# Kernel tuning notes

Hardware: AMD Instinct MI355X
Metric: run time of the kernel (lower is better)

The kernel has to match this reference:

```python
import jax, jax.numpy as jnp
import numpy as np

# Hardcoded in the torch module: interpolate to size=(32, 64) -> H=32, W=64
OUT_H, OUT_W = 32, 64
IGNORE_LABEL = 19
TAU = 0.07
EPS = 1e-12  # F.normalize eps


def _lin_idx(in_size, out_size):
    # torch bilinear, align_corners=False (default): half-pixel centers, clamped
    src = (jnp.arange(out_size, dtype=jnp.float32) + 0.5) * (in_size / out_size) - 0.5
    src = jnp.clip(src, 0.0, in_size - 1)
    i0 = jnp.floor(src).astype(jnp.int32)
    i1 = jnp.minimum(i0 + 1, in_size - 1)
    w = src - i0.astype(jnp.float32)
    return i0, i1, w


def bilinear_resize(x, Ho, Wo):
    # x: [B, C, Hi, Wi] -> [B, C, Ho, Wo], separable lerp
    Hi, Wi = x.shape[2], x.shape[3]
    h0, h1, wh = _lin_idx(Hi, Ho)
    w0, w1, ww = _lin_idx(Wi, Wo)
    wh = wh[None, None, :, None]
    xh = x[:, :, h0, :] * (1.0 - wh) + x[:, :, h1, :] * wh
    return xh[:, :, :, w0] * (1.0 - ww) + xh[:, :, :, w1] * ww


def nearest_resize_labels(lab, Ho, Wo):
    # torch 'nearest' (legacy): src = floor(dst * in/out)
    Hi, Wi = lab.shape[1], lab.shape[2]
    ih = jnp.floor(jnp.arange(Ho) * (Hi / Ho)).astype(jnp.int32)
    iw = jnp.floor(jnp.arange(Wo) * (Wi / Wo)).astype(jnp.int32)
    return lab[:, ih, :][:, :, iw]


def setup_inputs() -> dict:
    key = jax.random.key(0)
    k1, k2 = jax.random.split(key)
    features = jax.random.normal(k1, (8, 256, 128, 256), dtype=jnp.float32)
    labels = jax.random.randint(k2, (8, 128, 256), 0, 20, dtype=jnp.int32)
    return {"features": features, "labels": labels}


def reference(features, labels):
    # --- forward() ---
    f = bilinear_resize(features, OUT_H, OUT_W)               # [B, C, 32, 64]
    lab = nearest_resize_labels(labels, OUT_H, OUT_W)         # [B, 32, 64]
    lab = lab.astype(jnp.float32).reshape(lab.shape[0], -1)   # [B, N], N=2048

    B, C = f.shape[0], f.shape[1]
    f = f.reshape(B, C, -1).transpose(0, 2, 1)                # [B, N, C]
    f = f / jnp.maximum(jnp.linalg.norm(f, axis=2, keepdims=True), EPS)

    eq = (lab[:, :, None] == lab[:, None, :])                 # [B, N, N]
    ign = (lab == IGNORE_LABEL).astype(f.dtype)               # [B, N]
    weight_mask = eq.astype(f.dtype) * (1.0 - ign[:, :, None])
    ign_t = ign[:, None, :]                                   # ignore_mask_t (cols)

    logits = jnp.einsum('bnc,bmc->bnm', f, f) / TAU           # [B, N, N]
    # NOTE: original code computes a -1e9-masked copy but passes the UNMASKED
    # logits into supervised_contrastive_loss; we reproduce that faithfully.

    # --- supervised_contrastive_loss() ---
    p = jax.nn.softmax(logits, axis=2)
    p = p * (1.0 - ign_t) + ign_t                             # ignored cols -> 1 (log 0)
    ll = jnp.sum(-jnp.log(p) * weight_mask, axis=2)           # [B, N]
    den = jnp.sum(weight_mask, axis=2)                        # [B, N]
    ind = (den == 0).astype(f.dtype)
    den = den * (1.0 - ind) + ind
    ll = ll / den
    ll = jnp.where(jnp.isnan(ll), 0.0, ll)                    # nan -> 0
    index_sum = jnp.sum(1.0 - ind, axis=1)                    # [B]
    ind2 = (index_sum == 0).astype(f.dtype)
    index_sum = index_sum + ind2
    loss = jnp.mean(jnp.sum(ll, axis=1) / index_sum)
    return loss
```

## Files before the change

### kernel.cpp

```cpp
#include <hip/hip_runtime.h>
#include <math.h>

#define NB 8
#define NC 256
#define HI 128
#define WI 256
#define NN 2048
#define IGN 19
#define SQT 3.7796447300922722f

typedef _Float16 half8  __attribute__((ext_vector_type(8)));
typedef _Float16 half4v __attribute__((ext_vector_type(4)));
typedef float    f32x4  __attribute__((ext_vector_type(4)));

#define MFMA16(a, b, c) __builtin_amdgcn_mfma_f32_16x16x32_f16((a), (b), (c), 0, 0, 0)
#define GLOAD_LDS16(gp, lp) __builtin_amdgcn_global_load_lds( \
    (const __attribute__((address_space(1))) void*)(gp), \
    (__attribute__((address_space(3))) void*)(lp), 16, 0, 0)

__global__ void k_resize(const float* __restrict__ x, float* __restrict__ G) {
    int t = blockIdx.x * 256 + threadIdx.x;
    int j = t & 63;
    int i = (t >> 6) & 31;
    int c = (t >> 11) & 255;
    int b = t >> 19;
    const float* row = x + ((((size_t)b*NC + c)*HI + (4*i+1))*WI + 4*j);
    float4 r0 = *(const float4*)row;
    float4 r1 = *(const float4*)(row + WI);
    G[((size_t)b*NC + c)*NN + i*64 + j] = 0.25f*(r0.y + r0.z + r1.y + r1.z);
}

__global__ void k_labels(const int* __restrict__ lab, int* __restrict__ L,
                         int* __restrict__ hist) {
    int b = blockIdx.x;
    __shared__ int h[20];
    if (threadIdx.x < 20) h[threadIdx.x] = 0;
    __syncthreads();
    for (int n = threadIdx.x; n < NN; n += 256) {
        int i = n >> 6, j = n & 63;
        int v = lab[((size_t)b*HI + 4*i)*WI + 4*j];
        L[b*NN + n] = v;
        atomicAdd(&h[v], 1);
    }
    __syncthreads();
    if (threadIdx.x < 20) hist[b*20 + threadIdx.x] = h[threadIdx.x];
}

__global__ void k_norm(const float* __restrict__ G, float* __restrict__ invn) {
    int t = blockIdx.x * 256 + threadIdx.x;
    int b = t >> 11, n = t & 2047;
    const float* p = G + (size_t)b*NC*NN + n;
    float s = 0.f;
    #pragma unroll 8
    for (int c = 0; c < NC; c++) { float v = p[c*NN]; s += v*v; }
    invn[t] = 1.0f / fmaxf(sqrtf(s), 1e-12f);
}

__global__ void k_pack(const float* __restrict__ G, const float* __restrict__ invn,
                       _Float16* __restrict__ Phi, _Float16* __restrict__ Plo) {
    int blk = blockIdx.x;
    int b  = blk & 7;
    int t  = blk >> 3;
    int c0 = (t >> 5) * 64;
    int n0 = (t & 31) * 64;
    __shared__ float T[64][65];
    const float* Gb = G + (size_t)b*NC*NN;
    const float* invb = invn + b*NN;
    int tid = threadIdx.x;
    #pragma unroll
    for (int it = 0; it < 4; it++) {
        int idx = it*256 + tid;
        int cl = idx >> 4, nq = idx & 15;
        float4 v = *(const float4*)&Gb[(size_t)(c0+cl)*NN + n0 + nq*4];
        T[cl][nq*4+0]=v.x; T[cl][nq*4+1]=v.y; T[cl][nq*4+2]=v.z; T[cl][nq*4+3]=v.w;
    }
    __syncthreads();
    #pragma unroll
    for (int it = 0; it < 4; it++) {
        int idx = it*256 + tid;
        int nl = idx >> 4, cq = idx & 15;
        float s = invb[n0+nl] * SQT;
        half4v hh, hl;
        #pragma unroll
        for (int e = 0; e < 4; e++) {
            float v = T[cq*4+e][nl] * s;
            _Float16 h = (_Float16)v;
            hh[e] = h;
            hl[e] = (_Float16)(v - (float)h);
        }
        size_t o = ((size_t)(b*NN + n0 + nl))*NC + c0 + cq*4;
        *(half4v*)&Phi[o] = hh;
        *(half4v*)&Plo[o] = hl;
    }
}

__global__ __launch_bounds__(256, 1)
void k_main(const _Float16* __restrict__ Phi, const _Float16* __restrict__ Plo,
            const int* __restrict__ L, const int* __restrict__ hist,
            float* __restrict__ rowval) {
    int b    = blockIdx.x & 7;
    int tile = blockIdx.x >> 3;
    int n0   = tile * 64;
    const _Float16* PhiB = Phi + (size_t)b*NN*NC;
    const _Float16* PloB = Plo + (size_t)b*NN*NC;
    const int* Lb = L + b*NN;

    __shared__ _Float16 BhS[2][64*NC];
    __shared__ _Float16 BlS[2][64*NC];
    __shared__ float smM[2][64], smS[2][64], smMS[2][64];

    int tid  = threadIdx.x;
    int lane = tid & 63;
    int w    = tid >> 6;
    int wr   = w >> 1, wc = w & 1;
    int lr16 = lane & 15, lq = lane >> 4;

    half8 Ah[2][8], Al[2][8];
    #pragma unroll
    for (int t = 0; t < 2; t++) {
        int row = n0 + wr*32 + t*16 + lr16;
        const _Float16* pa = PhiB + (size_t)row*NC + lq*8;
        const _Float16* pb = PloB + (size_t)row*NC + lq*8;
        #pragma unroll
        for (int s = 0; s < 8; s++) {
            Ah[t][s] = *(const half8*)(pa + s*32);
            Al[t][s] = *(const half8*)(pb + s*32);
        }
    }
    int4 lr4[2];
    #pragma unroll
    for (int t = 0; t < 2; t++)
        lr4[t] = *(const int4*)&Lb[n0 + wr*32 + t*16 + lq*4];

    float sm_m[8], sm_s[8], sm_ms[8];
    #pragma unroll
    for (int i = 0; i < 8; i++) { sm_m[i] = -1e30f; sm_s[i] = 0.f; sm_ms[i] = 0.f; }

    auto stage = [&](int mt, int buf) {
        int mb = mt * 64;
        #pragma unroll
        for (int it = 0; it < 8; it++) {
            int ch  = w*512 + it*64 + lane;
            int col = ch >> 5, kbs = ch & 31;
            int src = (mb + col)*NC + ((kbs ^ (col & 7)) << 3);
            int dst = (w*512 + it*64) * 8;
            GLOAD_LDS16(PhiB + src, &BhS[buf][dst]);
            GLOAD_LDS16(PloB + src, &BlS[buf][dst]);
        }
    };

    auto compute = [&](int mt, int buf) {
        int mb  = mt * 64;
        int cl0 = wc*32 + lr16;
        int cl1 = cl0 + 16;
        int lc0 = Lb[mb + cl0];
        int lc1 = Lb[mb + cl1];
        f32x4 acc[2][2];
        #pragma unroll
        for (int t = 0; t < 2; t++)
            #pragma unroll
            for (int u = 0; u < 2; u++) acc[t][u] = (f32x4){0.f,0.f,0.f,0.f};

        #pragma unroll
        for (int s = 0; s < 8; s++) {
            int x0 = ((s*4 + lq) ^ (lr16 & 7)) << 3;
            half8 B0h = *(const half8*)&BhS[buf][cl0*NC + x0];
            half8 B1h = *(const half8*)&BhS[buf][cl1*NC + x0];
            half8 B0l = *(const half8*)&BlS[buf][cl0*NC + x0];
            half8 B1l = *(const half8*)&BlS[buf][cl1*NC + x0];
            #pragma unroll
            for (int t = 0; t < 2; t++) {
                acc[t][0] = MFMA16(Ah[t][s], B0h, acc[t][0]);
                acc[t][0] = MFMA16(Ah[t][s], B0l, acc[t][0]);
                acc[t][0] = MFMA16(Al[t][s], B0h, acc[t][0]);
                acc[t][1] = MFMA16(Ah[t][s], B1h, acc[t][1]);
                acc[t][1] = MFMA16(Ah[t][s], B1l, acc[t][1]);
                acc[t][1] = MFMA16(Al[t][s], B1h, acc[t][1]);
            }
        }
        #pragma unroll
        for (int t = 0; t < 2; t++) {
            int lrv[4] = {lr4[t].x, lr4[t].y, lr4[t].z, lr4[t].w};
            #pragma unroll
            for (int r = 0; r < 4; r++) {
                float v0 = acc[t][0][r], v1 = acc[t][1][r];
                int i = t*4 + r;
                float nm = fmaxf(sm_m[i], fmaxf(v0, v1));
                sm_s[i] = sm_s[i]*__expf(sm_m[i]-nm) + __expf(v0-nm) + __expf(v1-nm);
                sm_m[i] = nm;
                sm_ms[i] += (lc0 == lrv[r] ? v0 : 0.f) + (lc1 == lrv[r] ? v1 : 0.f);
            }
        }
    };

    stage(0, 0);
    __syncthreads();
    for (int mt = 0; mt < 32; mt++) {
        int cur = mt & 1;
        if (mt + 1 < 32) stage(mt + 1, cur ^ 1);
        compute(mt, cur);
        __syncthreads();
    }

    #pragma unroll
    for (int i = 0; i < 8; i++) {
        #pragma unroll
        for (int off = 1; off < 16; off <<= 1) {
            float om  = __shfl_xor(sm_m[i], off, 16);
            float os  = __shfl_xor(sm_s[i], off, 16);
            float oms = __shfl_xor(sm_ms[i], off, 16);
            float nm = fmaxf(sm_m[i], om);
            sm_s[i] = sm_s[i]*__expf(sm_m[i]-nm) + os*__expf(om-nm);
            sm_m[i] = nm;
            sm_ms[i] += oms;
        }
    }
    if (lr16 == 0) {
        #pragma unroll
        for (int t = 0; t < 2; t++)
            #pragma unroll
            for (int r = 0; r < 4; r++) {
                int rl = wr*32 + t*16 + lq*4 + r;
                smM[wc][rl]  = sm_m[t*4+r];
                smS[wc][rl]  = sm_s[t*4+r];
                smMS[wc][rl] = sm_ms[t*4+r];
            }
    }
    __syncthreads();
    if (tid < 64) {
        float m0 = smM[0][tid], m1 = smM[1][tid];
        float nm = fmaxf(m0, m1);
        float ss = smS[0][tid]*__expf(m0-nm) + smS[1][tid]*__expf(m1-nm);
        float msv = smMS[0][tid] + smMS[1][tid];
        int lrv = Lb[n0 + tid];
        float o = 0.f;
        if (lrv != IGN) {
            float den = (float)hist[b*20 + lrv];
            o = (nm + logf(ss)) - msv/den;
        }
        rowval[b*NN + n0 + tid] = o;
    }
}

__global__ void k_final(const float* __restrict__ rowval,
                        const int* __restrict__ hist, float* __restrict__ out) {
    __shared__ float red[4];
    int tid = threadIdx.x;
    float loss = 0.f;
    for (int b = 0; b < NB; b++) {
        float s = 0.f;
        for (int n = tid; n < NN; n += 256) s += rowval[b*NN + n];
        #pragma unroll
        for (int off = 32; off >= 1; off >>= 1) s += __shfl_down(s, off, 64);
        if ((tid & 63) == 0) red[tid >> 6] = s;
        __syncthreads();
        if (tid == 0) {
            float tot = red[0] + red[1] + red[2] + red[3];
            int cnt = NN - hist[b*20 + IGN];
            float isum = (cnt == 0) ? 1.f : (float)cnt;
            loss += tot / isum;
        }
        __syncthreads();
    }
    if (tid == 0) out[0] = loss / (float)NB;
}

extern "C" void kernel_launch(void* const* d_in, const int* in_sizes, int n_in,
                              void* d_out, int out_size, void* d_ws, size_t ws_size,
                              hipStream_t stream) {
    const float* x  = (const float*)d_in[0];
    const int* lab  = (const int*)d_in[1];
    float* out      = (float*)d_out;
    char* ws        = (char*)d_ws;

    const size_t G_BYTES = (size_t)NB*NC*NN*4;
    const size_t P_BYTES = (size_t)NB*NC*NN*2;
    float*     G      = (float*)ws;
    _Float16*  Phi    = (_Float16*)(ws + G_BYTES);
    _Float16*  Plo    = (_Float16*)(ws + G_BYTES + P_BYTES);
    float*     invn   = (float*)(ws + G_BYTES + 2*P_BYTES);
    float*     rowval = (float*)(ws + G_BYTES + 2*P_BYTES + 65536);
    int*       L      = (int*)  (ws + G_BYTES + 2*P_BYTES + 2*65536);
    int*       hist   = (int*)  (ws + G_BYTES + 2*P_BYTES + 3*65536);

    k_resize<<<NB*NC*NN/256, 256, 0, stream>>>(x, G);
    k_labels<<<NB, 256, 0, stream>>>(lab, L, hist);
    k_norm  <<<NB*NN/256, 256, 0, stream>>>(G, invn);
    k_pack  <<<NB*4*32, 256, 0, stream>>>(G, invn, Phi, Plo);
    k_main  <<<NB*(NN/64), 256, 0, stream>>>(Phi, Plo, L, hist, rowval);
    k_final <<<1, 256, 0, stream>>>(rowval, hist, out);
}
```

Before: 433.6 us.

## Fuse resize, norm and fp16 split-pack into one kernel; atomically reduce row losses

```diff
diff --git a/kernel.cpp b/kernel.cpp
--- a/kernel.cpp
+++ b/kernel.cpp
@@ -10,7 +10,6 @@
 #define SQT 3.7796447300922722f
 
 typedef _Float16 half8  __attribute__((ext_vector_type(8)));
-typedef _Float16 half4v __attribute__((ext_vector_type(4)));
 typedef float    f32x4  __attribute__((ext_vector_type(4)));
 
 #define MFMA16(a, b, c) __builtin_amdgcn_mfma_f32_16x16x32_f16((a), (b), (c), 0, 0, 0)
@@ -18,23 +17,12 @@
     (const __attribute__((address_space(1))) void*)(gp), \
     (__attribute__((address_space(3))) void*)(lp), 16, 0, 0)
 
-__global__ void k_resize(const float* __restrict__ x, float* __restrict__ G) {
-    int t = blockIdx.x * 256 + threadIdx.x;
-    int j = t & 63;
-    int i = (t >> 6) & 31;
-    int c = (t >> 11) & 255;
-    int b = t >> 19;
-    const float* row = x + ((((size_t)b*NC + c)*HI + (4*i+1))*WI + 4*j);
-    float4 r0 = *(const float4*)row;
-    float4 r1 = *(const float4*)(row + WI);
-    G[((size_t)b*NC + c)*NN + i*64 + j] = 0.25f*(r0.y + r0.z + r1.y + r1.z);
-}
-
 __global__ void k_labels(const int* __restrict__ lab, int* __restrict__ L,
-                         int* __restrict__ hist) {
+                         int* __restrict__ hist, float* __restrict__ accB) {
     int b = blockIdx.x;
     __shared__ int h[20];
     if (threadIdx.x < 20) h[threadIdx.x] = 0;
+    if (threadIdx.x == 0) accB[b] = 0.f;
     __syncthreads();
     for (int n = threadIdx.x; n < NN; n += 256) {
         int i = n >> 6, j = n & 63;
@@ -46,58 +34,64 @@
     if (threadIdx.x < 20) hist[b*20 + threadIdx.x] = h[threadIdx.x];
 }
 
-__global__ void k_norm(const float* __restrict__ G, float* __restrict__ invn) {
-    int t = blockIdx.x * 256 + threadIdx.x;
-    int b = t >> 11, n = t & 2047;
-    const float* p = G + (size_t)b*NC*NN + n;
-    float s = 0.f;
-    #pragma unroll 8
-    for (int c = 0; c < NC; c++) { float v = p[c*NN]; s += v*v; }
-    invn[t] = 1.0f / fmaxf(sqrtf(s), 1e-12f);
-}
-
-__global__ void k_pack(const float* __restrict__ G, const float* __restrict__ invn,
-                       _Float16* __restrict__ Phi, _Float16* __restrict__ Plo) {
+__global__ __launch_bounds__(512, 1)
+void k_fuse(const float* __restrict__ x, _Float16* __restrict__ Phi,
+            _Float16* __restrict__ Plo) {
     int blk = blockIdx.x;
-    int b  = blk & 7;
-    int t  = blk >> 3;
-    int c0 = (t >> 5) * 64;
-    int n0 = (t & 31) * 64;
-    __shared__ float T[64][65];
-    const float* Gb = G + (size_t)b*NC*NN;
-    const float* invb = invn + b*NN;
+    int b = blk & 7;
+    int i = blk >> 3;
+    __shared__ float V[NC][65];
+    __shared__ float nred[8][64];
+    __shared__ float invl[64];
     int tid = threadIdx.x;
+    int tc  = tid >> 6;
+    int j   = tid & 63;
+
+    float acc = 0.f;
+    #pragma unroll 4
+    for (int cc = 0; cc < 32; cc++) {
+        int c = tc*32 + cc;
+        const float* row = x + ((((size_t)b*NC + c)*HI + (4*i+1))*WI + 4*j);
+        float4 r0 = *(const float4*)row;
+        float4 r1 = *(const float4*)(row + WI);
+        float v = 0.25f*(r0.y + r0.z + r1.y + r1.z);
+        V[c][j] = v;
+        acc += v*v;
+    }
+    nred[tc][j] = acc;
+    __syncthreads();
+    if (tid < 64) {
+        float s = 0.f;
+        #pragma unroll
+        for (int q = 0; q < 8; q++) s += nred[q][tid];
+        invl[tid] = (1.0f / fmaxf(sqrtf(s), 1e-12f)) * SQT;
+    }
+    __syncthreads();
+
     #pragma unroll
     for (int it = 0; it < 4; it++) {
-        int idx = it*256 + tid;
-        int cl = idx >> 4, nq = idx & 15;
-        float4 v = *(const float4*)&Gb[(size_t)(c0+cl)*NN + n0 + nq*4];
-        T[cl][nq*4+0]=v.x; T[cl][nq*4+1]=v.y; T[cl][nq*4+2]=v.z; T[cl][nq*4+3]=v.w;
-    }
-    __syncthreads();
-    #pragma unroll
-    for (int it = 0; it < 4; it++) {
-        int idx = it*256 + tid;
-        int nl = idx >> 4, cq = idx & 15;
-        float s = invb[n0+nl] * SQT;
-        half4v hh, hl;
-        #pragma unroll
-        for (int e = 0; e < 4; e++) {
-            float v = T[cq*4+e][nl] * s;
+        int idx = it*512 + tid;
+        int nl = idx >> 5;
+        int ch = idx & 31;
+        float sc = invl[nl];
+        half8 hh, hl;
+        #pragma unroll
+        for (int e = 0; e < 8; e++) {
+            float v = V[ch*8+e][nl] * sc;
             _Float16 h = (_Float16)v;
             hh[e] = h;
             hl[e] = (_Float16)(v - (float)h);
         }
-        size_t o = ((size_t)(b*NN + n0 + nl))*NC + c0 + cq*4;
-        *(half4v*)&Phi[o] = hh;
-        *(half4v*)&Plo[o] = hl;
+        size_t o = ((size_t)(b*NN + i*64 + nl))*NC + ch*8;
+        *(half8*)&Phi[o] = hh;
+        *(half8*)&Plo[o] = hl;
     }
 }
 
 __global__ __launch_bounds__(256, 1)
 void k_main(const _Float16* __restrict__ Phi, const _Float16* __restrict__ Plo,
             const int* __restrict__ L, const int* __restrict__ hist,
-            float* __restrict__ rowval) {
+            float* __restrict__ accB) {
     int b    = blockIdx.x & 7;
     int tile = blockIdx.x >> 3;
     int n0   = tile * 64;
@@ -238,31 +232,23 @@
             float den = (float)hist[b*20 + lrv];
             o = (nm + logf(ss)) - msv/den;
         }
-        rowval[b*NN + n0 + tid] = o;
-    }
-}
-
-__global__ void k_final(const float* __restrict__ rowval,
+        #pragma unroll
+        for (int off = 32; off >= 1; off >>= 1) o += __shfl_down(o, off, 64);
+        if (tid == 0) atomicAdd(&accB[b], o);
+    }
+}
+
+__global__ void k_final(const float* __restrict__ accB,
                         const int* __restrict__ hist, float* __restrict__ out) {
-    __shared__ float red[4];
-    int tid = threadIdx.x;
-    float loss = 0.f;
-    for (int b = 0; b < NB; b++) {
-        float s = 0.f;
-        for (int n = tid; n < NN; n += 256) s += rowval[b*NN + n];
-        #pragma unroll
-        for (int off = 32; off >= 1; off >>= 1) s += __shfl_down(s, off, 64);
-        if ((tid & 63) == 0) red[tid >> 6] = s;
-        __syncthreads();
-        if (tid == 0) {
-            float tot = red[0] + red[1] + red[2] + red[3];
+    if (threadIdx.x == 0) {
+        float loss = 0.f;
+        for (int b = 0; b < NB; b++) {
             int cnt = NN - hist[b*20 + IGN];
             float isum = (cnt == 0) ? 1.f : (float)cnt;
-            loss += tot / isum;
-        }
-        __syncthreads();
-    }
-    if (tid == 0) out[0] = loss / (float)NB;
+            loss += accB[b] / isum;
+        }
+        out[0] = loss / (float)NB;
+    }
 }
 
 extern "C" void kernel_launch(void* const* d_in, const int* in_sizes, int n_in,
@@ -273,20 +259,15 @@
     float* out      = (float*)d_out;
     char* ws        = (char*)d_ws;
 
-    const size_t G_BYTES = (size_t)NB*NC*NN*4;
     const size_t P_BYTES = (size_t)NB*NC*NN*2;
-    float*     G      = (float*)ws;
-    _Float16*  Phi    = (_Float16*)(ws + G_BYTES);
-    _Float16*  Plo    = (_Float16*)(ws + G_BYTES + P_BYTES);
-    float*     invn   = (float*)(ws + G_BYTES + 2*P_BYTES);
-    float*     rowval = (float*)(ws + G_BYTES + 2*P_BYTES + 65536);
-    int*       L      = (int*)  (ws + G_BYTES + 2*P_BYTES + 2*65536);
-    int*       hist   = (int*)  (ws + G_BYTES + 2*P_BYTES + 3*65536);
-
-    k_resize<<<NB*NC*NN/256, 256, 0, stream>>>(x, G);
-    k_labels<<<NB, 256, 0, stream>>>(lab, L, hist);
-    k_norm  <<<NB*NN/256, 256, 0, stream>>>(G, invn);
-    k_pack  <<<NB*4*32, 256, 0, stream>>>(G, invn, Phi, Plo);
-    k_main  <<<NB*(NN/64), 256, 0, stream>>>(Phi, Plo, L, hist, rowval);
-    k_final <<<1, 256, 0, stream>>>(rowval, hist, out);
-}
+    _Float16*  Phi  = (_Float16*)ws;
+    _Float16*  Plo  = (_Float16*)(ws + P_BYTES);
+    int*       L    = (int*)  (ws + 2*P_BYTES);
+    int*       hist = (int*)  (ws + 2*P_BYTES + 65536);
+    float*     accB = (float*)(ws + 2*P_BYTES + 65536 + 4096);
+
+    k_labels<<<NB, 256, 0, stream>>>(lab, L, hist, accB);
+    k_fuse  <<<NB*32, 512, 0, stream>>>(x, Phi, Plo);
+    k_main  <<<NB*(NN/64), 256, 0, stream>>>(Phi, Plo, L, hist, accB);
+    k_final <<<1, 64, 0, stream>>>(accB, hist, out);
+}
```

Measured after the change: 397.2 us. -8.4%, faster.
